# Performance work log

Measured on AMD Instinct MI355X. Metric: run time of the kernel, lower is better.

## Reference

```python
import jax, jax.numpy as jnp
import numpy as np

H = 256  # hidden_size
B, LQ, LK = 4, 4096, 4096


def setup_inputs() -> dict:
    key = jax.random.key(0)
    ks = jax.random.split(key, 9)
    s = 1.0 / np.sqrt(H)
    return {
        "q": jax.random.normal(ks[0], (B, LQ, H), jnp.float32),
        "k": jax.random.normal(ks[1], (B, LK, H), jnp.float32),
        "v": jax.random.normal(ks[2], (B, LK, H), jnp.float32),
        "Wq": jax.random.uniform(ks[3], (H, H), jnp.float32, -s, s),
        "bq": jax.random.uniform(ks[4], (H,), jnp.float32, -s, s),
        "Wk": jax.random.uniform(ks[5], (H, H), jnp.float32, -s, s),
        "bk": jax.random.uniform(ks[6], (H,), jnp.float32, -s, s),
        "Wv": jax.random.uniform(ks[7], (H, H), jnp.float32, -s, s),
        "bv": jax.random.uniform(ks[8], (H,), jnp.float32, -s, s),
    }


def reference(q, k, v, Wq, bq, Wk, bk, Wv, bv):
    # Linear projections (torch Linear: x @ W.T + b)
    query = jnp.einsum('bsh,oh->bso', q, Wq) + bq
    keys = jnp.einsum('bsh,oh->bso', k, Wk) + bk
    values = jnp.einsum('bsh,oh->bso', v, Wv) + bv
    scores = jnp.einsum('bqh,bkh->bqk', query, keys) / jnp.sqrt(jnp.float32(H))
    weights = jax.nn.softmax(scores, axis=-1)
    context = jnp.einsum('bqk,bkh->bqh', weights, values)
    return context
```

## Files before the change

kernel.cpp:

```cpp
#include <hip/hip_runtime.h>
#include <hip/hip_bf16.h>
#include <stdint.h>

#define HD   256
#define SEQ  4096
#define NB   4
#define NTOK (NB * SEQ)
#define NEL  ((size_t)NTOK * HD)

typedef __hip_bfloat16 bf16;
typedef short    bf16x8  __attribute__((ext_vector_type(8)));
typedef float    f32x16  __attribute__((ext_vector_type(16)));
typedef float    f32x4_t __attribute__((ext_vector_type(4)));
typedef uint32_t u32x2_t __attribute__((ext_vector_type(2)));

__device__ __forceinline__ uint32_t pk2bf(float a, float b) {
  uint32_t ua = __builtin_bit_cast(uint32_t, a);
  uint32_t ub = __builtin_bit_cast(uint32_t, b);
  return ((ua + 0x8000u) >> 16) | ((ub + 0x8000u) & 0xFFFF0000u);
}
__device__ __forceinline__ uint16_t f2bf(float a) {
  uint32_t u = __builtin_bit_cast(uint32_t, a);
  return (uint16_t)((u + 0x8000u) >> 16);
}
__device__ __forceinline__ float bf2f(short s) {
  return __builtin_bit_cast(float, ((uint32_t)(uint16_t)s) << 16);
}

__global__ __launch_bounds__(256, 2) void proj_kernel(
    const float* __restrict__ Xq, const float* __restrict__ Xk, const float* __restrict__ Xv,
    const float* __restrict__ Wq, const float* __restrict__ Wk, const float* __restrict__ Wv,
    const float* __restrict__ bq, const float* __restrict__ bk, const float* __restrict__ bv,
    bf16* __restrict__ out0, float cexp) {
  const int which = (int)blockIdx.y;
  const float* X    = which == 0 ? Xq : which == 1 ? Xk : Xv;
  const float* W    = which == 0 ? Wq : which == 1 ? Wk : Wv;
  const float* bias = which == 0 ? bq : which == 1 ? bk : bv;
  const float scale = which == 0 ? cexp : 1.0f;

  __shared__ __align__(16) char praw[36864];
  bf16 (*xl)[264] = (bf16(*)[264])praw;

  const int tid = (int)threadIdx.x;
  const int w = tid >> 6, l = tid & 63;
  const int m = l & 31, h = l >> 5;
  const int m0 = (int)blockIdx.x * 64;

#pragma unroll
  for (int j = 0; j < 16; ++j) {
    int e = j * 256 + tid;
    int row = e >> 6, c4 = e & 63;
    f32x4_t v = *(const f32x4_t*)(X + (size_t)(m0 + row) * HD + c4 * 4);
    u32x2_t pk; pk.x = pk2bf(v.x, v.y); pk.y = pk2bf(v.z, v.w);
    *(u32x2_t*)(&xl[row][c4 * 4]) = pk;
  }
  __syncthreads();

  f32x16 acc00 = {}, acc01 = {}, acc10 = {}, acc11 = {};

#pragma unroll
  for (int kh = 0; kh < 2; ++kh) {
    bf16x8 bfr[2][8];
#pragma unroll
    for (int nt2 = 0; nt2 < 2; ++nt2)
#pragma unroll
      for (int ks = 0; ks < 8; ++ks) {
        const float* wp = W + (size_t)(w * 64 + nt2 * 32 + m) * HD + (kh * 8 + ks) * 16 + h * 8;
        f32x4_t w0 = *(const f32x4_t*)wp;
        f32x4_t w1 = *(const f32x4_t*)(wp + 4);
        union { uint32_t u[4]; bf16x8 v; } cv;
        cv.u[0] = pk2bf(w0.x, w0.y); cv.u[1] = pk2bf(w0.z, w0.w);
        cv.u[2] = pk2bf(w1.x, w1.y); cv.u[3] = pk2bf(w1.z, w1.w);
        bfr[nt2][ks] = cv.v;
      }
#pragma unroll
    for (int ks = 0; ks < 8; ++ks) {
      int kbyte = (kh * 8 + ks) * 32 + h * 16;
      bf16x8 a0 = *(const bf16x8*)((const char*)&xl[m][0] + kbyte);
      bf16x8 a1 = *(const bf16x8*)((const char*)&xl[32 + m][0] + kbyte);
      acc00 = __builtin_amdgcn_mfma_f32_32x32x16_bf16(a0, bfr[0][ks], acc00, 0, 0, 0);
      acc01 = __builtin_amdgcn_mfma_f32_32x32x16_bf16(a0, bfr[1][ks], acc01, 0, 0, 0);
      acc10 = __builtin_amdgcn_mfma_f32_32x32x16_bf16(a1, bfr[0][ks], acc10, 0, 0, 0);
      acc11 = __builtin_amdgcn_mfma_f32_32x32x16_bf16(a1, bfr[1][ks], acc11, 0, 0, 0);
    }
  }
  __syncthreads();

  float bv0 = bias[w * 64 + m];
  float bv1 = bias[w * 64 + 32 + m];

  if (which == 2) {
    bf16 (*lt)[72] = (bf16(*)[72])praw;
    const int n0 = w * 64 + m;
#pragma unroll
    for (int r2 = 0; r2 < 4; ++r2) {
      int tok = 8 * r2 + 4 * h;
      u32x2_t v0, v1, v2, v3;
      v0.x = pk2bf(acc00[r2 * 4 + 0] + bv0, acc00[r2 * 4 + 1] + bv0);
      v0.y = pk2bf(acc00[r2 * 4 + 2] + bv0, acc00[r2 * 4 + 3] + bv0);
      v1.x = pk2bf(acc01[r2 * 4 + 0] + bv1, acc01[r2 * 4 + 1] + bv1);
      v1.y = pk2bf(acc01[r2 * 4 + 2] + bv1, acc01[r2 * 4 + 3] + bv1);
      v2.x = pk2bf(acc10[r2 * 4 + 0] + bv0, acc10[r2 * 4 + 1] + bv0);
      v2.y = pk2bf(acc10[r2 * 4 + 2] + bv0, acc10[r2 * 4 + 3] + bv0);
      v3.x = pk2bf(acc11[r2 * 4 + 0] + bv1, acc11[r2 * 4 + 1] + bv1);
      v3.y = pk2bf(acc11[r2 * 4 + 2] + bv1, acc11[r2 * 4 + 3] + bv1);
      *(u32x2_t*)&lt[n0][tok]            = v0;
      *(u32x2_t*)&lt[n0 + 32][tok]       = v1;
      *(u32x2_t*)&lt[n0][32 + tok]       = v2;
      *(u32x2_t*)&lt[n0 + 32][32 + tok]  = v3;
    }
    __syncthreads();
    bf16* Vt = out0 + 2 * NEL;
    const int batch = m0 >> 12, sg = m0 & (SEQ - 1);
#pragma unroll
    for (int j = 0; j < 8; ++j) {
      int unit = j * 256 + tid;
      int r = unit >> 3, c = unit & 7;
      f32x4_t vv = *(const f32x4_t*)&lt[r][c * 8];
      *(f32x4_t*)(Vt + (size_t)batch * HD * SEQ + (size_t)r * SEQ + sg + c * 8) = vv;
    }
  } else {
    bf16* out = out0 + (size_t)which * NEL;
#pragma unroll
    for (int r = 0; r < 16; ++r) {
      int row = (r & 3) + ((r >> 2) << 3) + 4 * h;
      xl[row][w * 64 + m]           = __builtin_bit_cast(bf16, f2bf((acc00[r] + bv0) * scale));
      xl[row][w * 64 + 32 + m]      = __builtin_bit_cast(bf16, f2bf((acc01[r] + bv1) * scale));
      xl[32 + row][w * 64 + m]      = __builtin_bit_cast(bf16, f2bf((acc10[r] + bv0) * scale));
      xl[32 + row][w * 64 + 32 + m] = __builtin_bit_cast(bf16, f2bf((acc11[r] + bv1) * scale));
    }
    __syncthreads();
#pragma unroll
    for (int j = 0; j < 8; ++j) {
      int unit = j * 256 + tid;
      int row = unit >> 5, uc = unit & 31;
      f32x4_t vv = *(const f32x4_t*)((const char*)&xl[row][0] + uc * 16);
      *(f32x4_t*)(out + (size_t)(m0 + row) * HD + uc * 8) = vv;
    }
  }
}

__global__ __launch_bounds__(512, 2) void attn_kernel(
    const bf16* __restrict__ Qp, const bf16* __restrict__ Kp,
    const bf16* __restrict__ Vt, bf16* __restrict__ Op,
    float* __restrict__ Lp, int kvlen, int cpx) {
  __shared__ __align__(128) char smem[65536];
  char* Kl = smem;
  char* Vl = smem + 32768;

  const int tid = (int)threadIdx.x;
  const int w = tid >> 6, l = tid & 63;
  const int m = l & 31, h = l >> 5;

  int fid = (int)blockIdx.x + 16 * ((int)blockIdx.y + 4 * (int)blockIdx.z);
  int nid = (fid & 7) * cpx + (fid >> 3);
  const int qt = nid & 15, b = (nid >> 4) & 3, sp = nid >> 6;
  const int kvbase = sp * kvlen;
  const int niter = kvlen >> 5;

  const int gq = b * SEQ + qt * 256 + w * 32 + m;
  bf16x8 qf[16];
#pragma unroll
  for (int ks = 0; ks < 16; ++ks)
    qf[ks] = *(const bf16x8*)(Qp + (size_t)gq * HD + ks * 16 + h * 8);

  f32x16 oacc[8] = {};
  float Lacc = 0.f;

  auto stage = [&](int buf, int kv0) {
#pragma unroll
    for (int i = 0; i < 2; ++i) {
      int kk = i * 16 + w * 2 + (l >> 5);
      int s = (l & 31) ^ (kk & 31);
      const bf16* src = Kp + (size_t)(b * SEQ + kv0 + kk) * HD + s * 8;
      __builtin_amdgcn_global_load_lds(
          (const __attribute__((address_space(1))) void*)src,
          (__attribute__((address_space(3))) void*)(Kl + buf * 16384 + i * 8192 + w * 1024),
          16, 0, 0);
    }
#pragma unroll
    for (int i = 0; i < 2; ++i) {
      int r = i * 32 + w * 4 + (l >> 4);
      int x = (l & 15) ^ (r & 15);
      int d = (r << 2) + (x >> 2), j = x & 3;
      const bf16* src = Vt + (size_t)b * HD * SEQ + (size_t)d * SEQ + kv0 + j * 8;
      __builtin_amdgcn_global_load_lds(
          (const __attribute__((address_space(1))) void*)src,
          (__attribute__((address_space(3))) void*)(Vl + buf * 16384 + i * 8192 + w * 1024),
          16, 0, 0);
    }
  };

  stage(0, kvbase);

  for (int t = 0; t < niter; ++t) {
    const int cur = t & 1;

    asm volatile("s_barrier" ::: "memory");
    if (t + 1 < niter) {
      stage(cur ^ 1, kvbase + (t + 1) * 32);
      asm volatile("s_waitcnt vmcnt(4)" ::: "memory");
    } else {
      asm volatile("s_waitcnt vmcnt(0)" ::: "memory");
    }
    asm volatile("s_barrier" ::: "memory");

    f32x16 s0 = {};
    const char* kb = Kl + cur * 16384 + m * 512;
    __builtin_amdgcn_s_setprio(1);
#pragma unroll
    for (int ks = 0; ks < 16; ++ks) {
      bf16x8 k0 = *(const bf16x8*)(kb + (((2 * ks + h) ^ m) << 4));
      s0 = __builtin_amdgcn_mfma_f32_32x32x16_bf16(k0, qf[ks], s0, 0, 0, 0);
    }
    __builtin_amdgcn_s_setprio(0);

    float p[16];
#pragma unroll
    for (int r = 0; r < 16; ++r) p[r] = __builtin_exp2f(s0[r]);
    float ls = 0.f;
#pragma unroll
    for (int r = 0; r < 16; ++r) ls += p[r];
    Lacc += ls;

    bf16x8 pf[2];
#pragma unroll
    for (int ks = 0; ks < 2; ++ks) {
      int o = ks * 8;
      uint32_t P0, P1, P2, P3;
      asm("v_cvt_pk_bf16_f32 %0, %1, %2" : "=v"(P0) : "v"(p[o + 0]), "v"(p[o + 1]));
      asm("v_cvt_pk_bf16_f32 %0, %1, %2" : "=v"(P1) : "v"(p[o + 2]), "v"(p[o + 3]));
      asm("v_cvt_pk_bf16_f32 %0, %1, %2" : "=v"(P2) : "v"(p[o + 4]), "v"(p[o + 5]));
      asm("v_cvt_pk_bf16_f32 %0, %1, %2" : "=v"(P3) : "v"(p[o + 6]), "v"(p[o + 7]));
      asm volatile("v_permlane32_swap_b32 %0, %1" : "+v"(P0), "+v"(P2));
      asm volatile("v_permlane32_swap_b32 %0, %1" : "+v"(P1), "+v"(P3));
      union { uint32_t u[4]; bf16x8 v; } cv;
      cv.u[0] = P0; cv.u[1] = P1; cv.u[2] = P2; cv.u[3] = P3;
      pf[ks] = cv.v;
    }

    const char* vb = Vl + cur * 16384;
    __builtin_amdgcn_s_setprio(1);
#pragma unroll
    for (int dt = 0; dt < 8; ++dt) {
      int d = dt * 32 + m;
      int r = d >> 2;
#pragma unroll
      for (int ks = 0; ks < 2; ++ks) {
        int x = (((d & 3) << 2) | (2 * ks + h)) ^ (r & 15);
        bf16x8 vf = *(const bf16x8*)(vb + r * 256 + x * 16);
        oacc[dt] = __builtin_amdgcn_mfma_f32_32x32x16_bf16(vf, pf[ks], oacc[dt], 0, 0, 0);
      }
    }
    __builtin_amdgcn_s_setprio(0);
  }

  float Lrow = Lacc + __shfl_xor(Lacc, 32, 64);
  if (l < 32)
    Lp[(size_t)sp * NTOK + b * SEQ + qt * 256 + w * 32 + m] = Lrow;

#pragma unroll
  for (int half = 0; half < 4; ++half) {
    __syncthreads();
    if ((w >> 1) == half) {
      const int ql = (w & 1) * 32 + m;
#pragma unroll
      for (int dt = 0; dt < 8; ++dt)
#pragma unroll
        for (int rq = 0; rq < 4; ++rq) {
          int drow = dt * 32 + rq * 8 + 4 * h;
          f32x4_t vv;
          vv.x = oacc[dt][rq * 4 + 0]; vv.y = oacc[dt][rq * 4 + 1];
          vv.z = oacc[dt][rq * 4 + 2]; vv.w = oacc[dt][rq * 4 + 3];
          int slot = (drow >> 2) ^ (ql & 31);
          *(f32x4_t*)(smem + ql * 1024 + slot * 16) = vv;
        }
    }
    __syncthreads();
#pragma unroll
    for (int j = 0; j < 8; ++j) {
      int unit = j * 512 + tid;
      int qq = unit >> 6, sl = unit & 63;
      f32x4_t vv = *(const f32x4_t*)(smem + qq * 1024 + ((sl ^ (qq & 31)) << 4));
      u32x2_t pk; pk.x = pk2bf(vv.x, vv.y); pk.y = pk2bf(vv.z, vv.w);
      int gqq = b * SEQ + qt * 256 + half * 64 + qq;
      *(u32x2_t*)(Op + (size_t)sp * NEL + (size_t)gqq * HD + sl * 4) = pk;
    }
  }
}

__global__ __launch_bounds__(256, 2) void combine_kernel(
    const bf16* __restrict__ Op, const float* __restrict__ Lp,
    float* __restrict__ out, int nsplit) {
  size_t u = (size_t)blockIdx.x * 256 + threadIdx.x;
  int row = (int)(u >> 5);
  float a[8] = {};
  float Ls = 0.f;
  for (int s = 0; s < nsplit; ++s) {
    bf16x8 pv = ((const bf16x8*)Op)[u + (size_t)s * (NEL >> 3)];
#pragma unroll
    for (int i = 0; i < 8; ++i) a[i] += bf2f(pv[i]);
    Ls += Lp[(size_t)s * NTOK + row];
  }
  float inv = 1.f / Ls;
  f32x4_t lo, hi;
  lo.x = a[0] * inv; lo.y = a[1] * inv; lo.z = a[2] * inv; lo.w = a[3] * inv;
  hi.x = a[4] * inv; hi.y = a[5] * inv; hi.z = a[6] * inv; hi.w = a[7] * inv;
  ((f32x4_t*)out)[2 * u]     = lo;
  ((f32x4_t*)out)[2 * u + 1] = hi;
}

extern "C" void kernel_launch(void* const* d_in, const int* in_sizes, int n_in,
                              void* d_out, int out_size, void* d_ws, size_t ws_size,
                              hipStream_t stream) {
  (void)in_sizes; (void)n_in; (void)out_size;
  const float* q  = (const float*)d_in[0];
  const float* k  = (const float*)d_in[1];
  const float* v  = (const float*)d_in[2];
  const float* Wq = (const float*)d_in[3];
  const float* bq = (const float*)d_in[4];
  const float* Wk = (const float*)d_in[5];
  const float* bk = (const float*)d_in[6];
  const float* Wv = (const float*)d_in[7];
  const float* bv = (const float*)d_in[8];

  char* ws = (char*)d_ws;
  bf16* Qp  = (bf16*)ws;
  bf16* Kp  = Qp + NEL;
  bf16* Vt  = Qp + 2 * NEL;
  bf16* Opb = Qp + 3 * NEL;

  int nsplit = 1;
  for (int cand = 4; cand > 1; cand >>= 1) {
    size_t need = 3 * NEL * 2 + (size_t)cand * NEL * 2 + (size_t)cand * NTOK * 4;
    if (ws_size >= need) { nsplit = cand; break; }
  }
  float* Lp = (float*)(Opb + (size_t)nsplit * NEL);

  const float CEXP = 0.09016844f;

  proj_kernel<<<dim3(NTOK / 64, 3), 256, 0, stream>>>(q, k, v, Wq, Wk, Wv, bq, bk, bv, Qp, CEXP);
  attn_kernel<<<dim3(SEQ / 256, NB, nsplit), 512, 0, stream>>>(
      Qp, Kp, Vt, Opb, Lp, SEQ / nsplit, 8 * nsplit);
  combine_kernel<<<(int)(NEL / 8 / 256), 256, 0, stream>>>(Opb, Lp, (float*)d_out, nsplit);
}
```

Before: 124.0 us.

## Split attention waves into QK producer and PV consumer roles via LDS

Waves are paired: even waves compute QK^T scores and exp, writing bf16 probabilities to a double-buffered LDS region, and odd waves read them one iteration later to run the PV MFMAs. Each block now covers 128 queries instead of 256, the grid doubles, and V staging is delayed by one tile to match the consumer lag. The intent is to overlap softmax/exp work with PV matrix math across waves. The cost is an extra LDS round trip for P, more shared memory per block (80KB, which may limit occupancy), and half the waves doing each phase, so K/V are reloaded twice as often per query.

```diff
diff --git a/kernel.cpp b/kernel.cpp
--- a/kernel.cpp
+++ b/kernel.cpp
@@ -144,30 +144,35 @@
     const bf16* __restrict__ Qp, const bf16* __restrict__ Kp,
     const bf16* __restrict__ Vt, bf16* __restrict__ Op,
     float* __restrict__ Lp, int kvlen, int cpx) {
-  __shared__ __align__(128) char smem[65536];
+  __shared__ __align__(128) char smem[81920];
   char* Kl = smem;
   char* Vl = smem + 32768;
+  char* Pl = smem + 65536;
 
   const int tid = (int)threadIdx.x;
   const int w = tid >> 6, l = tid & 63;
   const int m = l & 31, h = l >> 5;
-
-  int fid = (int)blockIdx.x + 16 * ((int)blockIdx.y + 4 * (int)blockIdx.z);
+  const int role = w & 1, pair = w >> 1;
+
+  int fid = (int)blockIdx.x + 32 * ((int)blockIdx.y + 4 * (int)blockIdx.z);
   int nid = (fid & 7) * cpx + (fid >> 3);
-  const int qt = nid & 15, b = (nid >> 4) & 3, sp = nid >> 6;
+  const int qt = nid & 31, b = (nid >> 5) & 3, sp = nid >> 7;
   const int kvbase = sp * kvlen;
   const int niter = kvlen >> 5;
 
-  const int gq = b * SEQ + qt * 256 + w * 32 + m;
   bf16x8 qf[16];
-#pragma unroll
-  for (int ks = 0; ks < 16; ++ks)
-    qf[ks] = *(const bf16x8*)(Qp + (size_t)gq * HD + ks * 16 + h * 8);
+  if (role == 0) {
+    const int gq = b * SEQ + qt * 128 + pair * 32 + m;
+#pragma unroll
+    for (int ks = 0; ks < 16; ++ks)
+      qf[ks] = *(const bf16x8*)(Qp + (size_t)gq * HD + ks * 16 + h * 8);
+  }
 
   f32x16 oacc[8] = {};
   float Lacc = 0.f;
 
-  auto stage = [&](int buf, int kv0) {
+  auto stage_K = [&](int tt) {
+    int kv0 = kvbase + tt * 32, buf = tt & 1;
 #pragma unroll
     for (int i = 0; i < 2; ++i) {
       int kk = i * 16 + w * 2 + (l >> 5);
@@ -178,6 +183,9 @@
           (__attribute__((address_space(3))) void*)(Kl + buf * 16384 + i * 8192 + w * 1024),
           16, 0, 0);
     }
+  };
+  auto stage_V = [&](int tt) {
+    int kv0 = kvbase + tt * 32, buf = tt & 1;
 #pragma unroll
     for (int i = 0; i < 2; ++i) {
       int r = i * 32 + w * 4 + (l >> 4);
@@ -191,79 +199,110 @@
     }
   };
 
-  stage(0, kvbase);
+  stage_K(0);
 
   for (int t = 0; t < niter; ++t) {
     const int cur = t & 1;
 
+    asm volatile("s_waitcnt lgkmcnt(0)" ::: "memory");
     asm volatile("s_barrier" ::: "memory");
+
     if (t + 1 < niter) {
-      stage(cur ^ 1, kvbase + (t + 1) * 32);
+      stage_K(t + 1);
+      stage_V(t);
       asm volatile("s_waitcnt vmcnt(4)" ::: "memory");
     } else {
-      asm volatile("s_waitcnt vmcnt(0)" ::: "memory");
+      stage_V(t);
+      asm volatile("s_waitcnt vmcnt(2)" ::: "memory");
     }
     asm volatile("s_barrier" ::: "memory");
 
-    f32x16 s0 = {};
-    const char* kb = Kl + cur * 16384 + m * 512;
-    __builtin_amdgcn_s_setprio(1);
-#pragma unroll
-    for (int ks = 0; ks < 16; ++ks) {
-      bf16x8 k0 = *(const bf16x8*)(kb + (((2 * ks + h) ^ m) << 4));
-      s0 = __builtin_amdgcn_mfma_f32_32x32x16_bf16(k0, qf[ks], s0, 0, 0, 0);
-    }
-    __builtin_amdgcn_s_setprio(0);
-
-    float p[16];
-#pragma unroll
-    for (int r = 0; r < 16; ++r) p[r] = __builtin_exp2f(s0[r]);
-    float ls = 0.f;
-#pragma unroll
-    for (int r = 0; r < 16; ++r) ls += p[r];
-    Lacc += ls;
-
-    bf16x8 pf[2];
-#pragma unroll
-    for (int ks = 0; ks < 2; ++ks) {
-      int o = ks * 8;
-      uint32_t P0, P1, P2, P3;
-      asm("v_cvt_pk_bf16_f32 %0, %1, %2" : "=v"(P0) : "v"(p[o + 0]), "v"(p[o + 1]));
-      asm("v_cvt_pk_bf16_f32 %0, %1, %2" : "=v"(P1) : "v"(p[o + 2]), "v"(p[o + 3]));
-      asm("v_cvt_pk_bf16_f32 %0, %1, %2" : "=v"(P2) : "v"(p[o + 4]), "v"(p[o + 5]));
-      asm("v_cvt_pk_bf16_f32 %0, %1, %2" : "=v"(P3) : "v"(p[o + 6]), "v"(p[o + 7]));
-      asm volatile("v_permlane32_swap_b32 %0, %1" : "+v"(P0), "+v"(P2));
-      asm volatile("v_permlane32_swap_b32 %0, %1" : "+v"(P1), "+v"(P3));
-      union { uint32_t u[4]; bf16x8 v; } cv;
-      cv.u[0] = P0; cv.u[1] = P1; cv.u[2] = P2; cv.u[3] = P3;
-      pf[ks] = cv.v;
-    }
-
+    if (role == 0) {
+      f32x16 s0 = {};
+      const char* kb = Kl + cur * 16384 + m * 512;
+      __builtin_amdgcn_s_setprio(1);
+#pragma unroll
+      for (int ks = 0; ks < 16; ++ks) {
+        bf16x8 k0 = *(const bf16x8*)(kb + (((2 * ks + h) ^ m) << 4));
+        s0 = __builtin_amdgcn_mfma_f32_32x32x16_bf16(k0, qf[ks], s0, 0, 0, 0);
+      }
+      __builtin_amdgcn_s_setprio(0);
+
+      float p[16];
+#pragma unroll
+      for (int r = 0; r < 16; ++r) p[r] = __builtin_exp2f(s0[r]);
+      float ls = 0.f;
+#pragma unroll
+      for (int r = 0; r < 16; ++r) ls += p[r];
+      Lacc += ls;
+
+      char* pw = Pl + cur * 8192 + pair * 2048;
+#pragma unroll
+      for (int ks = 0; ks < 2; ++ks) {
+        int o = ks * 8;
+        uint32_t P0, P1, P2, P3;
+        asm("v_cvt_pk_bf16_f32 %0, %1, %2" : "=v"(P0) : "v"(p[o + 0]), "v"(p[o + 1]));
+        asm("v_cvt_pk_bf16_f32 %0, %1, %2" : "=v"(P1) : "v"(p[o + 2]), "v"(p[o + 3]));
+        asm("v_cvt_pk_bf16_f32 %0, %1, %2" : "=v"(P2) : "v"(p[o + 4]), "v"(p[o + 5]));
+        asm("v_cvt_pk_bf16_f32 %0, %1, %2" : "=v"(P3) : "v"(p[o + 6]), "v"(p[o + 7]));
+        asm volatile("v_permlane32_swap_b32 %0, %1" : "+v"(P0), "+v"(P2));
+        asm volatile("v_permlane32_swap_b32 %0, %1" : "+v"(P1), "+v"(P3));
+        union { uint32_t u[4]; bf16x8 v; } cv;
+        cv.u[0] = P0; cv.u[1] = P1; cv.u[2] = P2; cv.u[3] = P3;
+        *(bf16x8*)(pw + ks * 1024 + l * 16) = cv.v;
+      }
+    } else if (t) {
+      const char* pb = Pl + (cur ^ 1) * 8192 + pair * 2048;
+      bf16x8 pf0 = *(const bf16x8*)(pb + l * 16);
+      bf16x8 pf1 = *(const bf16x8*)(pb + 1024 + l * 16);
+      const char* vb = Vl + (cur ^ 1) * 16384;
+      __builtin_amdgcn_s_setprio(1);
+#pragma unroll
+      for (int dt = 0; dt < 8; ++dt) {
+        int d = dt * 32 + m;
+        int r = d >> 2;
+        int x0 = (((d & 3) << 2) | h) ^ (r & 15);
+        int x1 = (((d & 3) << 2) | (2 + h)) ^ (r & 15);
+        bf16x8 vf0 = *(const bf16x8*)(vb + r * 256 + x0 * 16);
+        oacc[dt] = __builtin_amdgcn_mfma_f32_32x32x16_bf16(vf0, pf0, oacc[dt], 0, 0, 0);
+        bf16x8 vf1 = *(const bf16x8*)(vb + r * 256 + x1 * 16);
+        oacc[dt] = __builtin_amdgcn_mfma_f32_32x32x16_bf16(vf1, pf1, oacc[dt], 0, 0, 0);
+      }
+      __builtin_amdgcn_s_setprio(0);
+    }
+  }
+
+  asm volatile("s_waitcnt lgkmcnt(0)" ::: "memory");
+  asm volatile("s_waitcnt vmcnt(0)" ::: "memory");
+  asm volatile("s_barrier" ::: "memory");
+  if (role == 1) {
+    const int cur = (niter - 1) & 1;
+    const char* pb = Pl + cur * 8192 + pair * 2048;
+    bf16x8 pf0 = *(const bf16x8*)(pb + l * 16);
+    bf16x8 pf1 = *(const bf16x8*)(pb + 1024 + l * 16);
     const char* vb = Vl + cur * 16384;
-    __builtin_amdgcn_s_setprio(1);
 #pragma unroll
     for (int dt = 0; dt < 8; ++dt) {
       int d = dt * 32 + m;
       int r = d >> 2;
-#pragma unroll
-      for (int ks = 0; ks < 2; ++ks) {
-        int x = (((d & 3) << 2) | (2 * ks + h)) ^ (r & 15);
-        bf16x8 vf = *(const bf16x8*)(vb + r * 256 + x * 16);
-        oacc[dt] = __builtin_amdgcn_mfma_f32_32x32x16_bf16(vf, pf[ks], oacc[dt], 0, 0, 0);
-      }
-    }
-    __builtin_amdgcn_s_setprio(0);
-  }
-
-  float Lrow = Lacc + __shfl_xor(Lacc, 32, 64);
-  if (l < 32)
-    Lp[(size_t)sp * NTOK + b * SEQ + qt * 256 + w * 32 + m] = Lrow;
-
-#pragma unroll
-  for (int half = 0; half < 4; ++half) {
+      int x0 = (((d & 3) << 2) | h) ^ (r & 15);
+      int x1 = (((d & 3) << 2) | (2 + h)) ^ (r & 15);
+      bf16x8 vf0 = *(const bf16x8*)(vb + r * 256 + x0 * 16);
+      oacc[dt] = __builtin_amdgcn_mfma_f32_32x32x16_bf16(vf0, pf0, oacc[dt], 0, 0, 0);
+      bf16x8 vf1 = *(const bf16x8*)(vb + r * 256 + x1 * 16);
+      oacc[dt] = __builtin_amdgcn_mfma_f32_32x32x16_bf16(vf1, pf1, oacc[dt], 0, 0, 0);
+    }
+  } else {
+    float Lrow = Lacc + __shfl_xor(Lacc, 32, 64);
+    if (l < 32)
+      Lp[(size_t)sp * NTOK + b * SEQ + qt * 128 + pair * 32 + m] = Lrow;
+  }
+
+#pragma unroll
+  for (int rr = 0; rr < 2; ++rr) {
     __syncthreads();
-    if ((w >> 1) == half) {
-      const int ql = (w & 1) * 32 + m;
+    if (role == 1 && (pair >> 1) == rr) {
+      const int ql = (pair & 1) * 32 + m;
 #pragma unroll
       for (int dt = 0; dt < 8; ++dt)
 #pragma unroll
@@ -283,7 +322,7 @@
       int qq = unit >> 6, sl = unit & 63;
       f32x4_t vv = *(const f32x4_t*)(smem + qq * 1024 + ((sl ^ (qq & 31)) << 4));
       u32x2_t pk; pk.x = pk2bf(vv.x, vv.y); pk.y = pk2bf(vv.z, vv.w);
-      int gqq = b * SEQ + qt * 256 + half * 64 + qq;
+      int gqq = b * SEQ + qt * 128 + rr * 64 + qq;
       *(u32x2_t*)(Op + (size_t)sp * NEL + (size_t)gqq * HD + sl * 4) = pk;
     }
   }
@@ -340,7 +379,7 @@
   const float CEXP = 0.09016844f;
 
   proj_kernel<<<dim3(NTOK / 64, 3), 256, 0, stream>>>(q, k, v, Wq, Wk, Wv, bq, bk, bv, Qp, CEXP);
-  attn_kernel<<<dim3(SEQ / 256, NB, nsplit), 512, 0, stream>>>(
-      Qp, Kp, Vt, Opb, Lp, SEQ / nsplit, 8 * nsplit);
+  attn_kernel<<<dim3(SEQ / 128, NB, nsplit), 512, 0, stream>>>(
+      Qp, Kp, Vt, Opb, Lp, SEQ / nsplit, 16 * nsplit);
   combine_kernel<<<(int)(NEL / 8 / 256), 256, 0, stream>>>(Opb, Lp, (float*)d_out, nsplit);
 }
```

Result: slower. 174.0 us (+40.3%).
